# Kernel tuning notes

Hardware: AMD Instinct MI355X
Metric: run time of the kernel (lower is better)

## Reference

```python
import jax, jax.numpy as jnp
import numpy as np

NUM_CODES = 4096
CODE_DIM = 256
COMMITMENT_COST = 0.25
EMA_DECAY = 0.99
EPS = 1e-5


def setup_inputs() -> dict:
    key = jax.random.key(0)
    k1, k2, k3 = jax.random.split(key, 3)
    z = jax.random.normal(k1, (32768, CODE_DIM), dtype=jnp.float32)
    # torch init is uniform(-1/K, 1/K); scale a normal similarly for realism
    weight = jax.random.uniform(k2, (NUM_CODES, CODE_DIM), dtype=jnp.float32,
                                minval=-1.0 / NUM_CODES, maxval=1.0 / NUM_CODES)
    ema_cluster_size = jnp.ones((NUM_CODES,), dtype=jnp.float32)
    ema_w = weight + 0.0  # buffer initialized as a clone of the weights
    del k3
    return {"z": z, "weight": weight, "ema_cluster_size": ema_cluster_size, "ema_w": ema_w}


def reference(z, weight, ema_cluster_size, ema_w):
    # ---- distances: ||z||^2 - 2 z E^T + ||E||^2  -> [N, K] ----
    z2 = jnp.sum(z * z, axis=-1, keepdims=True)              # [N, 1]
    e2 = jnp.sum(weight * weight, axis=-1)                   # [K]
    d = z2 - 2.0 * (z @ weight.T) + e2                       # [N, K]
    indices = jnp.argmin(d, axis=-1)                         # [N] int
    z_q = weight[indices]                                    # [N, D] gather

    # ---- EMA codebook update (training path, buffers are detached) ----
    counts = jax.ops.segment_sum(jnp.ones_like(indices, dtype=z.dtype), indices,
                                 num_segments=NUM_CODES)     # [K]
    dw = jax.ops.segment_sum(z, indices, num_segments=NUM_CODES)  # [K, D]
    new_cs = EMA_DECAY * ema_cluster_size + (1.0 - EMA_DECAY) * counts
    n = jnp.sum(new_cs)
    new_cs = (new_cs + EPS) / (n + NUM_CODES * EPS) * n      # Laplace smoothing
    new_ema_w = EMA_DECAY * ema_w + (1.0 - EMA_DECAY) * dw
    new_weight = new_ema_w / new_cs[:, None]

    # ---- commitment loss + straight-through estimator ----
    vq_loss = COMMITMENT_COST * jnp.mean((z - jax.lax.stop_gradient(z_q)) ** 2)
    z_q_ste = z + jax.lax.stop_gradient(z_q - z)

    return z_q_ste, indices, vq_loss, new_weight, new_cs, new_ema_w
```

## Files before the change

### kernel.cpp

```cpp
#include <hip/hip_runtime.h>
#include <hip/hip_bf16.h>

#define N_ROWS 32768
#define K_CODES 4096
#define D_DIM 256
#define CAP 128
#define MARGIN_T 1e-3f
#define SLOTS 8

#define WS_COUNTS    0
#define WS_LOSSP     16384
#define WS_IDX       147456
#define WS_Z2        278528
#define WS_E2        409600
#define WS_CCOUNT    425984
#define WS_STARTS    442368
#define WS_CURSOR    458752
#define WS_ROWS      475136
#define WS_DW        688128

#define DO_ZB        0
#define DO_WB        16777216
#define DO_CAND      18874368
#define DO_CNT8      35651584
#define DO_LMAX      36175872

typedef __attribute__((ext_vector_type(8)))  short bf16x8;
typedef __attribute__((ext_vector_type(16))) float f32x16;
typedef __attribute__((ext_vector_type(8)))  unsigned short us8;

__global__ void k1_norms(const float* __restrict__ z, const float* __restrict__ w,
                         float* __restrict__ z2, float* __restrict__ e2)
{
#pragma clang fp contract(off)
    int gid = blockIdx.x * blockDim.x + threadIdx.x;
    const float* row;
    float* outp;
    if (gid < N_ROWS) { row = z + (size_t)gid * D_DIM; outp = z2 + gid; }
    else if (gid < N_ROWS + K_CODES) { row = w + (size_t)(gid - N_ROWS) * D_DIM; outp = e2 + (gid - N_ROWS); }
    else return;

    float total = 0.0f;
    for (int half = 0; half < 2; half++) {
        const float* x = row + half * 128;
        float r[8];
#pragma unroll
        for (int j = 0; j < 8; j++) { float v = x[j]; r[j] = v * v; }
        for (int i = 8; i < 128; i += 8) {
#pragma unroll
            for (int j = 0; j < 8; j++) { float v = x[i + j]; r[j] += v * v; }
        }
        float s = ((r[0] + r[1]) + (r[2] + r[3])) + ((r[4] + r[5]) + (r[6] + r[7]));
        if (half == 0) total = s; else total = total + s;
    }
    *outp = total;
}

__device__ inline unsigned short f2b(float f) {
    __hip_bfloat16 h = __float2bfloat16(f);
    return *(unsigned short*)&h;
}

__global__ void kconv(const float* __restrict__ z, const float* __restrict__ w,
                      unsigned short* __restrict__ zb, unsigned short* __restrict__ wb)
{
    const int lane  = threadIdx.x & 63;
    const int gwave = blockIdx.x * 4 + (threadIdx.x >> 6);
    const int kk    = gwave & 7;
    const int row   = (gwave >> 3) * 64 + lane;
    const float* src;
    unsigned short* panel;
    int g;
    if (row < N_ROWS) {
        src   = z + (size_t)row * D_DIM;
        panel = zb + ((size_t)((row >> 8) * 8 + kk) << 13);
        g     = (row >> 5) & 7;
    } else {
        int c = row - N_ROWS;
        src   = w + (size_t)c * D_DIM;
        panel = wb + ((size_t)((c >> 8) * 8 + kk) << 13);
        g     = (c >> 5) & 7;
    }
    const int r31 = row & 31;
    const float* s0 = src + kk * 32;
#pragma unroll
    for (int s = 0; s < 2; s++)
#pragma unroll
        for (int h = 0; h < 2; h++) {
            float4 a = *(const float4*)(s0 + s * 16 + h * 8);
            float4 b = *(const float4*)(s0 + s * 16 + h * 8 + 4);
            us8 o;
            o[0] = f2b(a.x); o[1] = f2b(a.y); o[2] = f2b(a.z); o[3] = f2b(a.w);
            o[4] = f2b(b.x); o[5] = f2b(b.y); o[6] = f2b(b.z); o[7] = f2b(b.w);
            *(us8*)(panel + (((g * 2 + s) * 64 + h * 32 + r31) << 3)) = o;
        }
}

__device__ inline void gload16(const void* g, void* l)
{
    __builtin_amdgcn_global_load_lds(
        (const __attribute__((address_space(1))) unsigned int*)g,
        (__attribute__((address_space(3))) unsigned int*)l,
        16, 0, 0);
}

__global__ __launch_bounds__(512, 2) void k2_scan(
    const unsigned short* __restrict__ zb, const unsigned short* __restrict__ wb,
    unsigned char* __restrict__ cnt8, unsigned int* __restrict__ cand2,
    float* __restrict__ lmax)
{
    __shared__ char smem[65536];
    const int tid  = threadIdx.x;
    const int lane = tid & 63;
    const int wid  = tid >> 6;
    const int wm   = wid >> 2;
    const int wn   = wid & 3;
    const int m    = lane & 31;
    const int half = lane >> 5;

    const int r_hw = blockIdx.y * 16 + blockIdx.x;
    const int o    = (r_hw & 7) * 256 + (r_hw >> 3);
    const int cb   = o & 15;
    const int rb   = o >> 4;
    const int rowBase  = rb * 256;
    const int codeBase = cb * 256;

    auto stage = [&](int kk, int buf) {
        char* Ab = smem + buf * 32768;
        char* Bb = Ab + 16384;
        const unsigned short* Ap = wb + ((size_t)(cb * 8 + kk) << 13);
        const unsigned short* Bp = zb + ((size_t)(rb * 8 + kk) << 13);
#pragma unroll
        for (int i = 0; i < 2; i++) {
            gload16(Ap + (size_t)((i * 512 + tid) << 3), Ab + (size_t)(i * 512 + tid) * 16);
            gload16(Bp + (size_t)((i * 512 + tid) << 3), Bb + (size_t)(i * 512 + tid) * 16);
        }
    };

    f32x16 acc[4][2];
    {
        f32x16 zz = {};
#pragma unroll
        for (int ms = 0; ms < 4; ms++)
#pragma unroll
            for (int ns = 0; ns < 2; ns++) acc[ms][ns] = zz;
    }

    stage(0, 0);

    for (int kk = 0; kk < 8; kk++) {
        const int buf = kk & 1;
        __syncthreads();
        if (kk + 1 < 8) stage(kk + 1, buf ^ 1);
        const char* Ab = smem + buf * 32768;
        const char* Bb = Ab + 16384;
#pragma unroll
        for (int s = 0; s < 2; s++) {
            bf16x8 af[4], bfr[2];
#pragma unroll
            for (int ms = 0; ms < 4; ms++)
                af[ms] = *(const bf16x8*)(Ab + (size_t)(((wm * 4 + ms) * 2 + s) * 64 + lane) * 16);
#pragma unroll
            for (int ns = 0; ns < 2; ns++)
                bfr[ns] = *(const bf16x8*)(Bb + (size_t)(((wn * 2 + ns) * 2 + s) * 64 + lane) * 16);
#pragma unroll
            for (int ms = 0; ms < 4; ms++)
#pragma unroll
                for (int ns = 0; ns < 2; ns++)
                    acc[ms][ns] = __builtin_amdgcn_mfma_f32_32x32x16_bf16(
                        af[ms], bfr[ns], acc[ms][ns], 0, 0, 0);
        }
    }

    float tmax[2] = {-1e30f, -1e30f};
#pragma unroll
    for (int ms = 0; ms < 4; ms++)
#pragma unroll
        for (int ns = 0; ns < 2; ns++)
#pragma unroll
            for (int r = 0; r < 16; r++)
                tmax[ns] = fmaxf(tmax[ns], acc[ms][ns][r]);
#pragma unroll
    for (int ns = 0; ns < 2; ns++)
        tmax[ns] = fmaxf(tmax[ns], __shfl_xor(tmax[ns], 32));

    __syncthreads();
    float* rmx  = (float*)smem;
    int*   lcnt = (int*)(smem + 2048);
    if (lane < 32) {
        rmx[wm * 256 + wn * 64 + 0 * 32 + lane] = tmax[0];
        rmx[wm * 256 + wn * 64 + 1 * 32 + lane] = tmax[1];
    }
    if (tid < 256) lcnt[tid] = 0;
    __syncthreads();

    float thr[2];
#pragma unroll
    for (int ns = 0; ns < 2; ns++) {
        const int lr = wn * 64 + ns * 32 + m;
        thr[ns] = fmaxf(rmx[lr], rmx[256 + lr]) - MARGIN_T;
    }

#pragma unroll
    for (int ms = 0; ms < 4; ms++)
#pragma unroll
        for (int ns = 0; ns < 2; ns++)
#pragma unroll
            for (int r = 0; r < 16; r++) {
                float v = acc[ms][ns][r];
                if (v >= thr[ns]) {
                    const int lr = wn * 64 + ns * 32 + m;
                    int slot = atomicAdd(&lcnt[lr], 1);
                    if (slot < SLOTS) {
                        int code = codeBase + wm * 128 + ms * 32
                                 + ((r & 3) + 8 * (r >> 2) + 4 * half);
                        int b = __float_as_int(v);
                        unsigned key = (unsigned)b ^ ((unsigned)(b >> 31) | 0x80000000u);
                        unsigned entry = (key & 0xFFFFF000u) | (unsigned)code;
                        cand2[((size_t)(rowBase + lr) * 16 + cb) * SLOTS + slot] = entry;
                    }
                }
            }

    __syncthreads();
    if (tid < 256) {
        int cf = lcnt[tid];
        cnt8[(size_t)(rowBase + tid) * 16 + cb] =
            (cf > SLOTS) ? (unsigned char)255 : (unsigned char)cf;
        lmax[(size_t)(rowBase + tid) * 16 + cb] = fmaxf(rmx[tid], rmx[256 + tid]);
    }
}

__global__ __launch_bounds__(256) void k_rescore(
    const float* __restrict__ z, const float* __restrict__ w,
    const float* __restrict__ z2, const float* __restrict__ e2,
    const unsigned char* __restrict__ cnt8, const unsigned int* __restrict__ cand2,
    const float* __restrict__ lmax, int* __restrict__ idx_out)
{
#pragma clang fp contract(off)
    const int lane = threadIdx.x & 63;
    const int wv   = threadIdx.x >> 6;
    const int n    = blockIdx.x * 4 + wv;

    __shared__ float4 zst[4][64];
    __shared__ int    surv[4][CAP];

    zst[wv][lane] = ((const float4*)(z + (size_t)n * D_DIM))[lane];

    int   c  = 0;
    float lm = -1e30f;
    if (lane < 16) {
        c  = cnt8[(size_t)n * 16 + lane];
        lm = lmax[(size_t)n * 16 + lane];
    }
    float gm = lm;
#pragma unroll
    for (int off = 32; off > 0; off >>= 1)
        gm = fmaxf(gm, __shfl_xor(gm, off));

    unsigned long long obal =
        __ballot((lane < 16) && (c == 255) && (lm >= gm - MARGIN_T));

    float bd = __builtin_inff(); int bk = K_CODES;
    const float z2v = z2[n];

    {
        const unsigned e0 = cand2[(size_t)n * 128 + lane];
        const unsigned e1 = cand2[(size_t)n * 128 + 64 + lane];
        const int craw0 = __shfl(c, lane >> 3);
        const int craw1 = __shfl(c, 8 + (lane >> 3));
        const int cl0 = (craw0 == 255) ? SLOTS : craw0;
        const int cl1 = (craw1 == 255) ? SLOTS : craw1;
        const float thrF = gm - MARGIN_T - 1e-4f;

        auto keyf = [](unsigned e) -> float {
            unsigned ky = e & 0xFFFFF000u;
            int b = (ky & 0x80000000u) ? (int)(ky ^ 0x80000000u) : (int)~ky;
            return __int_as_float(b);
        };
        const bool keep0 = ((lane & 7) < cl0) && (keyf(e0) >= thrF);
        const bool keep1 = ((lane & 7) < cl1) && (keyf(e1) >= thrF);

        unsigned long long bal0 = __ballot(keep0);
        unsigned long long bal1 = __ballot(keep1);
        const unsigned long long below = (1ull << lane) - 1ull;
        const int n0 = (int)__popcll(bal0);
        if (keep0) surv[wv][(int)__popcll(bal0 & below)] = (int)(e0 & 0xFFFu);
        if (keep1) surv[wv][n0 + (int)__popcll(bal1 & below)] = (int)(e1 & 0xFFFu);
        const int nt = n0 + (int)__popcll(bal1);

        for (int s = lane; s < nt; s += 64) {
            int k = surv[wv][s];
            if ((unsigned)k >= (unsigned)K_CODES) k = 0;
            const float4* wp = (const float4*)(w + (size_t)k * D_DIM);
            float tacc = 0.0f;
#pragma unroll 8
            for (int d4 = 0; d4 < 64; d4++) {
                float4 wvv = wp[d4];
                float4 zv  = zst[wv][d4];
                tacc = __builtin_fmaf(zv.x, wvv.x, tacc);
                tacc = __builtin_fmaf(zv.y, wvv.y, tacc);
                tacc = __builtin_fmaf(zv.z, wvv.z, tacc);
                tacc = __builtin_fmaf(zv.w, wvv.w, tacc);
            }
            float u  = z2v - 2.0f * tacc;
            float dv = u + e2[k];
            if (dv < bd || (dv == bd && k < bk)) { bd = dv; bk = k; }
        }
    }

    while (obal) {
        const int cbq = (int)(__ffsll((long long)obal) - 1);
        obal &= obal - 1ull;
        const int k0 = cbq * 256 + lane;
        const float4* w0 = (const float4*)(w + (size_t)(k0      ) * D_DIM);
        const float4* w1 = (const float4*)(w + (size_t)(k0 +  64) * D_DIM);
        const float4* w2 = (const float4*)(w + (size_t)(k0 + 128) * D_DIM);
        const float4* w3 = (const float4*)(w + (size_t)(k0 + 192) * D_DIM);
        float t0 = 0.0f, t1 = 0.0f, t2 = 0.0f, t3 = 0.0f;
#pragma unroll 8
        for (int d4 = 0; d4 < 64; d4++) {
            float4 zv = zst[wv][d4];
            float4 a0 = w0[d4];
            float4 a1 = w1[d4];
            float4 a2 = w2[d4];
            float4 a3 = w3[d4];
            t0 = __builtin_fmaf(zv.x, a0.x, t0);
            t1 = __builtin_fmaf(zv.x, a1.x, t1);
            t2 = __builtin_fmaf(zv.x, a2.x, t2);
            t3 = __builtin_fmaf(zv.x, a3.x, t3);
            t0 = __builtin_fmaf(zv.y, a0.y, t0);
            t1 = __builtin_fmaf(zv.y, a1.y, t1);
            t2 = __builtin_fmaf(zv.y, a2.y, t2);
            t3 = __builtin_fmaf(zv.y, a3.y, t3);
            t0 = __builtin_fmaf(zv.z, a0.z, t0);
            t1 = __builtin_fmaf(zv.z, a1.z, t1);
            t2 = __builtin_fmaf(zv.z, a2.z, t2);
            t3 = __builtin_fmaf(zv.z, a3.z, t3);
            t0 = __builtin_fmaf(zv.w, a0.w, t0);
            t1 = __builtin_fmaf(zv.w, a1.w, t1);
            t2 = __builtin_fmaf(zv.w, a2.w, t2);
            t3 = __builtin_fmaf(zv.w, a3.w, t3);
        }
        float d0 = (z2v - 2.0f * t0) + e2[k0];
        float d1 = (z2v - 2.0f * t1) + e2[k0 + 64];
        float d2 = (z2v - 2.0f * t2) + e2[k0 + 128];
        float d3 = (z2v - 2.0f * t3) + e2[k0 + 192];
        if (d0 < bd || (d0 == bd && k0       < bk)) { bd = d0; bk = k0; }
        if (d1 < bd || (d1 == bd && k0 +  64 < bk)) { bd = d1; bk = k0 + 64; }
        if (d2 < bd || (d2 == bd && k0 + 128 < bk)) { bd = d2; bk = k0 + 128; }
        if (d3 < bd || (d3 == bd && k0 + 192 < bk)) { bd = d3; bk = k0 + 192; }
    }

#pragma unroll
    for (int off = 1; off < 64; off <<= 1) {
        float od = __shfl_xor(bd, off);
        int   ok = __shfl_xor(bk, off);
        if (od < bd || (od == bd && ok < bk)) { bd = od; bk = ok; }
    }
    if (lane == 0) idx_out[n] = (bk < K_CODES) ? bk : 0;
}

__global__ void k_hist(const int* __restrict__ idx_in, int* __restrict__ ccount)
{
    int n = blockIdx.x * 256 + threadIdx.x;
    int idx = idx_in[n];
    if (idx < 0) idx = 0;
    if (idx >= K_CODES) idx = K_CODES - 1;
    atomicAdd(&ccount[idx], 1);
}

__global__ void k_prefix(const int* __restrict__ ccount,
                         int* __restrict__ starts, int* __restrict__ cursor)
{
    __shared__ int s[1024];
    const int t = threadIdx.x;
    int c0 = ccount[t * 4 + 0];
    int c1 = ccount[t * 4 + 1];
    int c2 = ccount[t * 4 + 2];
    int c3 = ccount[t * 4 + 3];
    int tsum = ((c0 + c1) + (c2 + c3));
    s[t] = tsum;
    __syncthreads();
    for (int off = 1; off < 1024; off <<= 1) {
        int v = (t >= off) ? s[t - off] : 0;
        __syncthreads();
        s[t] += v;
        __syncthreads();
    }
    int base = s[t] - tsum;
    starts[t * 4 + 0] = base;
    starts[t * 4 + 1] = base + c0;
    starts[t * 4 + 2] = base + c0 + c1;
    starts[t * 4 + 3] = base + c0 + c1 + c2;
    cursor[t * 4 + 0] = base;
    cursor[t * 4 + 1] = base + c0;
    cursor[t * 4 + 2] = base + c0 + c1;
    cursor[t * 4 + 3] = base + c0 + c1 + c2;
}

__global__ void k_fill(const int* __restrict__ idx_in, int* __restrict__ cursor,
                       int* __restrict__ rows)
{
    int n = blockIdx.x * 256 + threadIdx.x;
    int idx = idx_in[n];
    if (idx < 0) idx = 0;
    if (idx >= K_CODES) idx = K_CODES - 1;
    int pos = atomicAdd(&cursor[idx], 1);
    rows[pos] = n;
}

__global__ void k3_scatter(const float* __restrict__ z, const float* __restrict__ w,
                           const int* __restrict__ idx_in,
                           float* __restrict__ lossp, float* __restrict__ out_zq,
                           float* __restrict__ out_idx)
{
#pragma clang fp contract(off)
    const int n = blockIdx.x;
    const int t = threadIdx.x;
    int idx = idx_in[n];
    if (idx < 0) idx = 0;
    if (idx >= K_CODES) idx = K_CODES - 1;
    if (t == 0) out_idx[n] = (float)idx;

    float zv = z[(size_t)n * D_DIM + t];
    float wq = w[(size_t)idx * D_DIM + t];
    out_zq[(size_t)n * D_DIM + t] = zv + (wq - zv);
    float df = zv - wq;
    float sq = df * df;

    __shared__ float red[256];
    red[t] = sq; __syncthreads();
    for (int s = 128; s > 0; s >>= 1) {
        if (t < s) red[t] += red[t + s];
        __syncthreads();
    }
    if (t == 0) lossp[n] = red[0];
}

__global__ void k4_cs(const float* __restrict__ lossp, const int* __restrict__ ccount,
                      const float* __restrict__ cs_in, float* __restrict__ out_loss,
                      float* __restrict__ out_cs)
{
#pragma clang fp contract(off)
    const int t = threadIdx.x;
    __shared__ float red[1024];
    __shared__ float pre[K_CODES];

    float s = 0.0f;
    for (int i = t; i < N_ROWS; i += 1024) s += lossp[i];
    red[t] = s; __syncthreads();
    for (int st = 512; st > 0; st >>= 1) {
        if (t < st) red[t] += red[t + st];
        __syncthreads();
    }
    if (t == 0) out_loss[0] = 0.25f * (red[0] / 8388608.0f);
    __syncthreads();

    const float DEC = 0.99f;
    const float OMD = (float)(1.0 - 0.99);
    float mine[4];
#pragma unroll
    for (int q = 0; q < 4; q++) {
        int k = t + q * 1024;
        float t1 = DEC * cs_in[k];
        float t2 = OMD * (float)ccount[k];
        float p = t1 + t2;
        pre[k] = p; mine[q] = p;
    }
    float psum = (mine[0] + mine[1]) + (mine[2] + mine[3]);
    red[t] = psum; __syncthreads();
    for (int st = 512; st > 0; st >>= 1) {
        if (t < st) red[t] += red[t + st];
        __syncthreads();
    }
    float nsum = red[0];
    const float KEPS = (float)(4096.0 * 1e-5);
    float denom = nsum + KEPS;
#pragma unroll
    for (int q = 0; q < 4; q++) {
        int k = t + q * 1024;
        float v = ((pre[k] + 1e-5f) / denom) * nsum;
        out_cs[k] = v;
    }
}

__global__ void k5_emaw(const float* __restrict__ z, const float* __restrict__ ema_w,
                        const int* __restrict__ starts, const int* __restrict__ ccount,
                        const int* __restrict__ rows, const float* __restrict__ newcs,
                        float* __restrict__ out_w, float* __restrict__ out_emaw)
{
#pragma clang fp contract(off)
    const int k = blockIdx.x;
    const int t = threadIdx.x;
    const int s = starts[k];
    const int e = s + ccount[k];

    float acc = 0.0f;
    for (int r = s; r < e; r++) {
        int row = rows[r];
        acc += z[(size_t)row * D_DIM + t];
    }

    const float OMD = (float)(1.0 - 0.99);
    float t1 = 0.99f * ema_w[(size_t)k * D_DIM + t];
    float t2 = OMD * acc;
    float ne = t1 + t2;
    out_emaw[(size_t)k * D_DIM + t] = ne;
    out_w[(size_t)k * D_DIM + t] = ne / newcs[k];
}

extern "C" void kernel_launch(void* const* d_in, const int* in_sizes, int n_in,
                              void* d_out, int out_size, void* d_ws, size_t ws_size,
                              hipStream_t stream)
{
    const float* z    = (const float*)d_in[0];
    const float* w    = (const float*)d_in[1];
    const float* cs   = (const float*)d_in[2];
    const float* emaw = (const float*)d_in[3];

    float* out      = (float*)d_out;
    float* out_zq   = out;
    float* out_idx  = out + 8388608;
    float* out_loss = out + 8421376;
    float* out_w    = out + 8421377;
    float* out_cs   = out + 9469953;
    float* out_emaw = out + 9474049;

    char* ws = (char*)d_ws;
    float*          lossp   = (float*)(ws + WS_LOSSP);
    int*            idx_int = (int*)  (ws + WS_IDX);
    float*          z2      = (float*)(ws + WS_Z2);
    float*          e2      = (float*)(ws + WS_E2);
    int*            ccount  = (int*)  (ws + WS_CCOUNT);
    int*            starts  = (int*)  (ws + WS_STARTS);
    int*            cursor  = (int*)  (ws + WS_CURSOR);
    int*            rowsb   = (int*)  (ws + WS_ROWS);

    char* ob = (char*)d_out;
    unsigned short* zb    = (unsigned short*)(ob + DO_ZB);
    unsigned short* wb    = (unsigned short*)(ob + DO_WB);
    unsigned int*   cand2 = (unsigned int*)  (ob + DO_CAND);
    unsigned char*  cnt8  = (unsigned char*) (ob + DO_CNT8);
    float*          lmx   = (float*)         (ob + DO_LMAX);

    hipMemsetAsync(ccount, 0, K_CODES * sizeof(int), stream);

    k1_norms<<<(N_ROWS + K_CODES) / 256, 256, 0, stream>>>(z, w, z2, e2);

    kconv<<<1152, 256, 0, stream>>>(z, w, zb, wb);

    dim3 g2(16, 128);
    k2_scan<<<g2, 512, 0, stream>>>(zb, wb, cnt8, cand2, lmx);

    k_rescore<<<N_ROWS / 4, 256, 0, stream>>>(z, w, z2, e2, cnt8, cand2, lmx, idx_int);

    k_hist<<<N_ROWS / 256, 256, 0, stream>>>(idx_int, ccount);
    k_prefix<<<1, 1024, 0, stream>>>(ccount, starts, cursor);
    k_fill<<<N_ROWS / 256, 256, 0, stream>>>(idx_int, cursor, rowsb);

    k3_scatter<<<N_ROWS, 256, 0, stream>>>(z, w, idx_int, lossp, out_zq, out_idx);

    k4_cs<<<1, 1024, 0, stream>>>(lossp, ccount, cs, out_loss, out_cs);

    k5_emaw<<<K_CODES, 256, 0, stream>>>(z, emaw, starts, ccount, rowsb,
                                         out_cs, out_w, out_emaw);
}
```

Before: 381.4 us.

## Fuse small kernels to cut launches and use wave-per-row scatter

Merges the norm and bf16 conversion kernels into one launch split by block index. The histogram atomic moves into the rescore kernel, and the prefix scan is fused with the loss and cluster-size reduction kernel. The scatter kernel is rewritten to handle one row per 64-lane wave with float4 loads and a shuffle reduction, replacing one 256-thread block per row with a shared-memory tree. This removes several launches and barrier-heavy reductions, at the cost of a larger single-block kernel that serialises more work.

```diff
diff --git a/kernel.cpp b/kernel.cpp
--- a/kernel.cpp
+++ b/kernel.cpp
@@ -8,7 +8,6 @@
 #define MARGIN_T 1e-3f
 #define SLOTS 8
 
-#define WS_COUNTS    0
 #define WS_LOSSP     16384
 #define WS_IDX       147456
 #define WS_Z2        278528
@@ -17,7 +16,6 @@
 #define WS_STARTS    442368
 #define WS_CURSOR    458752
 #define WS_ROWS      475136
-#define WS_DW        688128
 
 #define DO_ZB        0
 #define DO_WB        16777216
@@ -29,71 +27,71 @@
 typedef __attribute__((ext_vector_type(16))) float f32x16;
 typedef __attribute__((ext_vector_type(8)))  unsigned short us8;
 
-__global__ void k1_norms(const float* __restrict__ z, const float* __restrict__ w,
-                         float* __restrict__ z2, float* __restrict__ e2)
-{
-#pragma clang fp contract(off)
-    int gid = blockIdx.x * blockDim.x + threadIdx.x;
-    const float* row;
-    float* outp;
-    if (gid < N_ROWS) { row = z + (size_t)gid * D_DIM; outp = z2 + gid; }
-    else if (gid < N_ROWS + K_CODES) { row = w + (size_t)(gid - N_ROWS) * D_DIM; outp = e2 + (gid - N_ROWS); }
-    else return;
-
-    float total = 0.0f;
-    for (int half = 0; half < 2; half++) {
-        const float* x = row + half * 128;
-        float r[8];
-#pragma unroll
-        for (int j = 0; j < 8; j++) { float v = x[j]; r[j] = v * v; }
-        for (int i = 8; i < 128; i += 8) {
-#pragma unroll
-            for (int j = 0; j < 8; j++) { float v = x[i + j]; r[j] += v * v; }
-        }
-        float s = ((r[0] + r[1]) + (r[2] + r[3])) + ((r[4] + r[5]) + (r[6] + r[7]));
-        if (half == 0) total = s; else total = total + s;
-    }
-    *outp = total;
-}
-
 __device__ inline unsigned short f2b(float f) {
     __hip_bfloat16 h = __float2bfloat16(f);
     return *(unsigned short*)&h;
 }
 
-__global__ void kconv(const float* __restrict__ z, const float* __restrict__ w,
-                      unsigned short* __restrict__ zb, unsigned short* __restrict__ wb)
-{
-    const int lane  = threadIdx.x & 63;
-    const int gwave = blockIdx.x * 4 + (threadIdx.x >> 6);
-    const int kk    = gwave & 7;
-    const int row   = (gwave >> 3) * 64 + lane;
-    const float* src;
-    unsigned short* panel;
-    int g;
-    if (row < N_ROWS) {
-        src   = z + (size_t)row * D_DIM;
-        panel = zb + ((size_t)((row >> 8) * 8 + kk) << 13);
-        g     = (row >> 5) & 7;
+__global__ void k1_kconv(const float* __restrict__ z, const float* __restrict__ w,
+                         float* __restrict__ z2, float* __restrict__ e2,
+                         unsigned short* __restrict__ zb, unsigned short* __restrict__ wb)
+{
+#pragma clang fp contract(off)
+    if (blockIdx.x < 145) {
+        int gid = blockIdx.x * blockDim.x + threadIdx.x;
+        const float* row;
+        float* outp;
+        if (gid < N_ROWS) { row = z + (size_t)gid * D_DIM; outp = z2 + gid; }
+        else if (gid < N_ROWS + K_CODES) { row = w + (size_t)(gid - N_ROWS) * D_DIM; outp = e2 + (gid - N_ROWS); }
+        else return;
+
+        float total = 0.0f;
+        for (int half = 0; half < 2; half++) {
+            const float* x = row + half * 128;
+            float r[8];
+#pragma unroll
+            for (int j = 0; j < 8; j++) { float v = x[j]; r[j] = v * v; }
+            for (int i = 8; i < 128; i += 8) {
+#pragma unroll
+                for (int j = 0; j < 8; j++) { float v = x[i + j]; r[j] += v * v; }
+            }
+            float s = ((r[0] + r[1]) + (r[2] + r[3])) + ((r[4] + r[5]) + (r[6] + r[7]));
+            if (half == 0) total = s; else total = total + s;
+        }
+        *outp = total;
     } else {
-        int c = row - N_ROWS;
-        src   = w + (size_t)c * D_DIM;
-        panel = wb + ((size_t)((c >> 8) * 8 + kk) << 13);
-        g     = (c >> 5) & 7;
-    }
-    const int r31 = row & 31;
-    const float* s0 = src + kk * 32;
-#pragma unroll
-    for (int s = 0; s < 2; s++)
-#pragma unroll
-        for (int h = 0; h < 2; h++) {
-            float4 a = *(const float4*)(s0 + s * 16 + h * 8);
-            float4 b = *(const float4*)(s0 + s * 16 + h * 8 + 4);
-            us8 o;
-            o[0] = f2b(a.x); o[1] = f2b(a.y); o[2] = f2b(a.z); o[3] = f2b(a.w);
-            o[4] = f2b(b.x); o[5] = f2b(b.y); o[6] = f2b(b.z); o[7] = f2b(b.w);
-            *(us8*)(panel + (((g * 2 + s) * 64 + h * 32 + r31) << 3)) = o;
+        const int bid   = blockIdx.x - 145;
+        const int lane  = threadIdx.x & 63;
+        const int gwave = bid * 4 + (threadIdx.x >> 6);
+        const int kk    = gwave & 7;
+        const int row   = (gwave >> 3) * 64 + lane;
+        const float* src;
+        unsigned short* panel;
+        int g;
+        if (row < N_ROWS) {
+            src   = z + (size_t)row * D_DIM;
+            panel = zb + ((size_t)((row >> 8) * 8 + kk) << 13);
+            g     = (row >> 5) & 7;
+        } else {
+            int c = row - N_ROWS;
+            src   = w + (size_t)c * D_DIM;
+            panel = wb + ((size_t)((c >> 8) * 8 + kk) << 13);
+            g     = (c >> 5) & 7;
         }
+        const int r31 = row & 31;
+        const float* s0 = src + kk * 32;
+#pragma unroll
+        for (int s = 0; s < 2; s++)
+#pragma unroll
+            for (int h = 0; h < 2; h++) {
+                float4 a = *(const float4*)(s0 + s * 16 + h * 8);
+                float4 b = *(const float4*)(s0 + s * 16 + h * 8 + 4);
+                us8 o;
+                o[0] = f2b(a.x); o[1] = f2b(a.y); o[2] = f2b(a.z); o[3] = f2b(a.w);
+                o[4] = f2b(b.x); o[5] = f2b(b.y); o[6] = f2b(b.z); o[7] = f2b(b.w);
+                *(us8*)(panel + (((g * 2 + s) * 64 + h * 32 + r31) << 3)) = o;
+            }
+    }
 }
 
 __device__ inline void gload16(const void* g, void* l)
@@ -235,7 +233,8 @@
     const float* __restrict__ z, const float* __restrict__ w,
     const float* __restrict__ z2, const float* __restrict__ e2,
     const unsigned char* __restrict__ cnt8, const unsigned int* __restrict__ cand2,
-    const float* __restrict__ lmax, int* __restrict__ idx_out)
+    const float* __restrict__ lmax, int* __restrict__ idx_out,
+    int* __restrict__ ccount)
 {
 #pragma clang fp contract(off)
     const int lane = threadIdx.x & 63;
@@ -358,23 +357,72 @@
         int   ok = __shfl_xor(bk, off);
         if (od < bd || (od == bd && ok < bk)) { bd = od; bk = ok; }
     }
-    if (lane == 0) idx_out[n] = (bk < K_CODES) ? bk : 0;
-}
-
-__global__ void k_hist(const int* __restrict__ idx_in, int* __restrict__ ccount)
-{
-    int n = blockIdx.x * 256 + threadIdx.x;
+    if (lane == 0) {
+        const int fk = (bk < K_CODES && bk >= 0) ? bk : 0;
+        idx_out[n] = fk;
+        atomicAdd(&ccount[fk], 1);
+    }
+}
+
+__global__ __launch_bounds__(256) void k3_scatter(
+    const float* __restrict__ z, const float* __restrict__ w,
+    const int* __restrict__ idx_in,
+    float* __restrict__ lossp, float* __restrict__ out_zq,
+    float* __restrict__ out_idx)
+{
+#pragma clang fp contract(off)
+    const int lane = threadIdx.x & 63;
+    const int wv   = threadIdx.x >> 6;
+    const int n    = blockIdx.x * 4 + wv;
+
     int idx = idx_in[n];
     if (idx < 0) idx = 0;
     if (idx >= K_CODES) idx = K_CODES - 1;
-    atomicAdd(&ccount[idx], 1);
-}
-
-__global__ void k_prefix(const int* __restrict__ ccount,
-                         int* __restrict__ starts, int* __restrict__ cursor)
-{
-    __shared__ int s[1024];
+
+    float4 zv = ((const float4*)(z + (size_t)n   * D_DIM))[lane];
+    float4 wq = ((const float4*)(w + (size_t)idx * D_DIM))[lane];
+
+    float4 q;
+    q.x = zv.x + (wq.x - zv.x);
+    q.y = zv.y + (wq.y - zv.y);
+    q.z = zv.z + (wq.z - zv.z);
+    q.w = zv.w + (wq.w - zv.w);
+    ((float4*)(out_zq + (size_t)n * D_DIM))[lane] = q;
+
+    float dx = zv.x - wq.x, dy = zv.y - wq.y, dz = zv.z - wq.z, dwc = zv.w - wq.w;
+    float sq = ((dx * dx + dy * dy) + (dz * dz + dwc * dwc));
+#pragma unroll
+    for (int off = 1; off < 64; off <<= 1)
+        sq += __shfl_xor(sq, off);
+
+    if (lane == 0) {
+        out_idx[n] = (float)idx;
+        lossp[n]   = sq;
+    }
+}
+
+__global__ void k_prefix_cs(const float* __restrict__ lossp,
+                            const int* __restrict__ ccount,
+                            const float* __restrict__ cs_in,
+                            int* __restrict__ starts, int* __restrict__ cursor,
+                            float* __restrict__ out_loss, float* __restrict__ out_cs)
+{
+#pragma clang fp contract(off)
     const int t = threadIdx.x;
+    __shared__ float red[1024];
+    __shared__ float pre[K_CODES];
+    __shared__ int   s[1024];
+
+    float sacc = 0.0f;
+    for (int i = t; i < N_ROWS; i += 1024) sacc += lossp[i];
+    red[t] = sacc; __syncthreads();
+    for (int st = 512; st > 0; st >>= 1) {
+        if (t < st) red[t] += red[t + st];
+        __syncthreads();
+    }
+    if (t == 0) out_loss[0] = 0.25f * (red[0] / 8388608.0f);
+    __syncthreads();
+
     int c0 = ccount[t * 4 + 0];
     int c1 = ccount[t * 4 + 1];
     int c2 = ccount[t * 4 + 2];
@@ -397,6 +445,33 @@
     cursor[t * 4 + 1] = base + c0;
     cursor[t * 4 + 2] = base + c0 + c1;
     cursor[t * 4 + 3] = base + c0 + c1 + c2;
+
+    const float DEC = 0.99f;
+    const float OMD = (float)(1.0 - 0.99);
+    float mine[4];
+#pragma unroll
+    for (int q = 0; q < 4; q++) {
+        int k = t + q * 1024;
+        float t1 = DEC * cs_in[k];
+        float t2 = OMD * (float)ccount[k];
+        float p = t1 + t2;
+        pre[k] = p; mine[q] = p;
+    }
+    float psum = (mine[0] + mine[1]) + (mine[2] + mine[3]);
+    red[t] = psum; __syncthreads();
+    for (int st = 512; st > 0; st >>= 1) {
+        if (t < st) red[t] += red[t + st];
+        __syncthreads();
+    }
+    float nsum = red[0];
+    const float KEPS = (float)(4096.0 * 1e-5);
+    float denom = nsum + KEPS;
+#pragma unroll
+    for (int q = 0; q < 4; q++) {
+        int k = t + q * 1024;
+        float v = ((pre[k] + 1e-5f) / denom) * nsum;
+        out_cs[k] = v;
+    }
 }
 
 __global__ void k_fill(const int* __restrict__ idx_in, int* __restrict__ cursor,
@@ -408,81 +483,6 @@
     if (idx >= K_CODES) idx = K_CODES - 1;
     int pos = atomicAdd(&cursor[idx], 1);
     rows[pos] = n;
-}
-
-__global__ void k3_scatter(const float* __restrict__ z, const float* __restrict__ w,
-                           const int* __restrict__ idx_in,
-                           float* __restrict__ lossp, float* __restrict__ out_zq,
-                           float* __restrict__ out_idx)
-{
-#pragma clang fp contract(off)
-    const int n = blockIdx.x;
-    const int t = threadIdx.x;
-    int idx = idx_in[n];
-    if (idx < 0) idx = 0;
-    if (idx >= K_CODES) idx = K_CODES - 1;
-    if (t == 0) out_idx[n] = (float)idx;
-
-    float zv = z[(size_t)n * D_DIM + t];
-    float wq = w[(size_t)idx * D_DIM + t];
-    out_zq[(size_t)n * D_DIM + t] = zv + (wq - zv);
-    float df = zv - wq;
-    float sq = df * df;
-
-    __shared__ float red[256];
-    red[t] = sq; __syncthreads();
-    for (int s = 128; s > 0; s >>= 1) {
-        if (t < s) red[t] += red[t + s];
-        __syncthreads();
-    }
-    if (t == 0) lossp[n] = red[0];
-}
-
-__global__ void k4_cs(const float* __restrict__ lossp, const int* __restrict__ ccount,
-                      const float* __restrict__ cs_in, float* __restrict__ out_loss,
-                      float* __restrict__ out_cs)
-{
-#pragma clang fp contract(off)
-    const int t = threadIdx.x;
-    __shared__ float red[1024];
-    __shared__ float pre[K_CODES];
-
-    float s = 0.0f;
-    for (int i = t; i < N_ROWS; i += 1024) s += lossp[i];
-    red[t] = s; __syncthreads();
-    for (int st = 512; st > 0; st >>= 1) {
-        if (t < st) red[t] += red[t + st];
-        __syncthreads();
-    }
-    if (t == 0) out_loss[0] = 0.25f * (red[0] / 8388608.0f);
-    __syncthreads();
-
-    const float DEC = 0.99f;
-    const float OMD = (float)(1.0 - 0.99);
-    float mine[4];
-#pragma unroll
-    for (int q = 0; q < 4; q++) {
-        int k = t + q * 1024;
-        float t1 = DEC * cs_in[k];
-        float t2 = OMD * (float)ccount[k];
-        float p = t1 + t2;
-        pre[k] = p; mine[q] = p;
-    }
-    float psum = (mine[0] + mine[1]) + (mine[2] + mine[3]);
-    red[t] = psum; __syncthreads();
-    for (int st = 512; st > 0; st >>= 1) {
-        if (t < st) red[t] += red[t + st];
-        __syncthreads();
-    }
-    float nsum = red[0];
-    const float KEPS = (float)(4096.0 * 1e-5);
-    float denom = nsum + KEPS;
-#pragma unroll
-    for (int q = 0; q < 4; q++) {
-        int k = t + q * 1024;
-        float v = ((pre[k] + 1e-5f) / denom) * nsum;
-        out_cs[k] = v;
-    }
 }
 
 __global__ void k5_emaw(const float* __restrict__ z, const float* __restrict__ ema_w,
@@ -546,22 +546,21 @@
 
     hipMemsetAsync(ccount, 0, K_CODES * sizeof(int), stream);
 
-    k1_norms<<<(N_ROWS + K_CODES) / 256, 256, 0, stream>>>(z, w, z2, e2);
-
-    kconv<<<1152, 256, 0, stream>>>(z, w, zb, wb);
+    k1_kconv<<<1297, 256, 0, stream>>>(z, w, z2, e2, zb, wb);
 
     dim3 g2(16, 128);
     k2_scan<<<g2, 512, 0, stream>>>(zb, wb, cnt8, cand2, lmx);
 
-    k_rescore<<<N_ROWS / 4, 256, 0, stream>>>(z, w, z2, e2, cnt8, cand2, lmx, idx_int);
-
-    k_hist<<<N_ROWS / 256, 256, 0, stream>>>(idx_int, ccount);
-    k_prefix<<<1, 1024, 0, stream>>>(ccount, starts, cursor);
+    k_rescore<<<N_ROWS / 4, 256, 0, stream>>>(z, w, z2, e2, cnt8, cand2, lmx,
+                                              idx_int, ccount);
+
+    k3_scatter<<<N_ROWS / 4, 256, 0, stream>>>(z, w, idx_int, lossp,
+                                               out_zq, out_idx);
+
+    k_prefix_cs<<<1, 1024, 0, stream>>>(lossp, ccount, cs, starts, cursor,
+                                        out_loss, out_cs);
+
     k_fill<<<N_ROWS / 256, 256, 0, stream>>>(idx_int, cursor, rowsb);
-
-    k3_scatter<<<N_ROWS, 256, 0, stream>>>(z, w, idx_int, lossp, out_zq, out_idx);
-
-    k4_cs<<<1, 1024, 0, stream>>>(lossp, ccount, cs, out_loss, out_cs);
 
     k5_emaw<<<K_CODES, 256, 0, stream>>>(z, emaw, starts, ccount, rowsb,
                                          out_cs, out_w, out_emaw);
```

Result: faster. 368.3 us (-3.4%).
